# Performance work log

Measured on AMD Instinct MI355X. Metric: run time of the kernel, lower is better.

## Reference

```python
import jax, jax.numpy as jnp
import numpy as np

VOC, EMB, HID = 32000, 512, 1024
B, S = 16, 256


def setup_inputs() -> dict:
    key = jax.random.key(0)
    ks = jax.random.split(key, 12)
    s_e = 1.0 / np.sqrt(HID)
    inp = {
        "inputs": jax.random.randint(ks[0], (B, S), 0, VOC, dtype=jnp.int64),
        "emb": jax.random.normal(ks[1], (VOC, EMB), dtype=jnp.float32),
        "W_ih1": jax.random.uniform(ks[2], (4 * HID, EMB), minval=-s_e, maxval=s_e),
        "W_hh1": jax.random.uniform(ks[3], (4 * HID, HID), minval=-s_e, maxval=s_e),
        "b_ih1": jax.random.uniform(ks[4], (4 * HID,), minval=-s_e, maxval=s_e),
        "b_hh1": jax.random.uniform(ks[5], (4 * HID,), minval=-s_e, maxval=s_e),
        "W_ih2": jax.random.uniform(ks[6], (4 * HID, HID), minval=-s_e, maxval=s_e),
        "W_hh2": jax.random.uniform(ks[7], (4 * HID, HID), minval=-s_e, maxval=s_e),
        "b_ih2": jax.random.uniform(ks[8], (4 * HID,), minval=-s_e, maxval=s_e),
        "b_hh2": jax.random.uniform(ks[9], (4 * HID,), minval=-s_e, maxval=s_e),
        "W_log": jax.random.uniform(ks[10], (VOC, HID), minval=-s_e, maxval=s_e),
        "b_log": jnp.zeros((VOC,), dtype=jnp.float32),  # init_weights zeroes logits bias
    }
    return inp


def _lstm_cell(x, h, c, W_ih, W_hh, b_ih, b_hh):
    # PyTorch LSTMCell: gates ordered (i, f, g, o)
    g = x @ W_ih.T + b_ih + h @ W_hh.T + b_hh  # [B, 4H]
    i, f, gg, o = jnp.split(g, 4, axis=-1)
    c_new = jax.nn.sigmoid(f) * c + jax.nn.sigmoid(i) * jnp.tanh(gg)
    h_new = jax.nn.sigmoid(o) * jnp.tanh(c_new)
    return h_new, c_new


def reference(inputs, emb, W_ih1, W_hh1, b_ih1, b_hh1,
              W_ih2, W_hh2, b_ih2, b_hh2, W_log, b_log):
    # Dropout is evaluated in inference mode (identity), for determinism.
    embed = emb[inputs]  # [B, S, E]
    xs = jnp.swapaxes(embed, 0, 1)  # [S, B, E]
    bsz = inputs.shape[0]
    h1 = jnp.zeros((bsz, HID), embed.dtype)
    c1 = jnp.zeros((bsz, HID), embed.dtype)
    h2 = jnp.zeros((bsz, HID), embed.dtype)
    c2 = jnp.zeros((bsz, HID), embed.dtype)

    def step(carry, x_t):
        h1, c1, h2, c2 = carry
        h1, c1 = _lstm_cell(x_t, h1, c1, W_ih1, W_hh1, b_ih1, b_hh1)
        h2, c2 = _lstm_cell(h1, h2, c2, W_ih2, W_hh2, b_ih2, b_hh2)
        return (h1, c1, h2, c2), h2

    _, hid_seq = jax.lax.scan(step, (h1, c1, h2, c2), xs)  # [S, B, H]
    hid_seq = jnp.swapaxes(hid_seq, 0, 1)  # [B, S, H]
    logits = hid_seq @ W_log.T + b_log  # [B, S, V]
    return jax.nn.log_softmax(logits, axis=-1)
```

## Files before the change

### kernel.cpp

```cpp
#include <hip/hip_runtime.h>
#include <hip/hip_bf16.h>

typedef __attribute__((ext_vector_type(8))) _Float16 half8;
typedef __attribute__((ext_vector_type(4))) _Float16 half4;
typedef __attribute__((ext_vector_type(4))) float f32x4;
typedef __attribute__((ext_vector_type(4))) unsigned int u32x4;

#define VOC 32000
#define EMB 512
#define HID 1024
#define SS  256
#define NROW 4096
#define CHK 43
#define CSTRIDE 64
#define SLOTB (64 * CSTRIDE * 16)
#define NS 4
#define SPIN (1 << 16)
#define ROWH 264

__device__ __forceinline__ float sigf(float x) {
    return 1.f / (1.f + __expf(-x));
}
__device__ __forceinline__ float tanh_c(float x) {
    x = fminf(fmaxf(x, -15.f), 15.f);
    float e = __expf(2.f * x);
    return (e - 1.f) / (e + 1.f);
}

__device__ __forceinline__ u32x4 ldg_u4_cc(const void* p) {
    u32x4 r;
    asm volatile("global_load_dwordx4 %0, %1, off sc0 sc1" : "=v"(r) : "v"(p));
    return r;
}
__device__ __forceinline__ void stg_u4_cc(void* p, u32x4 v) {
    asm volatile("global_store_dwordx4 %0, %1, off sc0 sc1" :: "v"(p), "v"(v) : "memory");
}
__device__ __forceinline__ void stg_u32_cc(unsigned* p, unsigned v) {
    asm volatile("global_store_dword %0, %1, off sc0 sc1" :: "v"(p), "v"(v) : "memory");
}
__device__ __forceinline__ unsigned ldg_u32_cc(const unsigned* p) {
    unsigned v;
    asm volatile("global_load_dword %0, %1, off sc0 sc1\n\ts_waitcnt vmcnt(0)"
                 : "=v"(v) : "v"(p) : "memory");
    return v;
}
__device__ __forceinline__ half8 to_agpr(half8 v) {
    asm volatile("" : "+a"(v));
    return v;
}
__device__ __forceinline__ void gload16(const void* g, void* lds) {
    __builtin_amdgcn_global_load_lds(
        (const __attribute__((address_space(1))) unsigned int*)(uintptr_t)g,
        (__attribute__((address_space(3))) unsigned int*)(unsigned int)(uintptr_t)lds,
        16, 0, 0);
}

__global__ void k_zero(float* p, int n) {
    int i = blockIdx.x * blockDim.x + threadIdx.x;
    int st = gridDim.x * blockDim.x;
    for (; i < n; i += st) p[i] = 0.f;
}

__global__ void k_f32_to_f16(const float* __restrict__ src,
                             _Float16* __restrict__ dst, int n4) {
    int i = blockIdx.x * blockDim.x + threadIdx.x;
    int st = gridDim.x * blockDim.x;
    for (; i < n4; i += st) {
        float4 v = ((const float4*)src)[i];
        half4 o = {(_Float16)v.x, (_Float16)v.y, (_Float16)v.z, (_Float16)v.w};
        ((half4*)dst)[i] = o;
    }
}

__global__ void k_bias(const float* bi1, const float* bh1,
                       const float* bi2, const float* bh2,
                       float* b1, float* b2) {
    int i = blockIdx.x * blockDim.x + threadIdx.x;
    if (i < 4 * HID) { b1[i] = bi1[i] + bh1[i]; b2[i] = bi2[i] + bh2[i]; }
}

__global__ void k_embed(const int* __restrict__ tok, const float* __restrict__ emb,
                        _Float16* __restrict__ A) {
    int idx = blockIdx.x * 256 + threadIdx.x;
    if (idx >= NROW * (EMB / 4)) return;
    int r = idx >> 7, c4 = idx & 127;
    int t = r >> 4, b = r & 15;
    int token = tok[b * SS + t];
    float4 v = ((const float4*)(emb + (size_t)token * EMB))[c4];
    half4 o = {(_Float16)v.x, (_Float16)v.y, (_Float16)v.z, (_Float16)v.w};
    ((half4*)(A + (size_t)r * EMB))[c4] = o;
}

template <int F16OUT>
__global__ __launch_bounds__(256) void k_gemm_bt(
    const _Float16* __restrict__ A, const _Float16* __restrict__ B,
    const float* __restrict__ bias, float* __restrict__ C,
    _Float16* __restrict__ Ch, int M, int N, int K, int scatter, int swz) {
    __shared__ __align__(16) _Float16 As[128 * 32];
    __shared__ __align__(16) _Float16 Bs[128 * 32];
    int tid = threadIdx.x;
    int wave = tid >> 6, lane = tid & 63;
    int nbx = gridDim.x;
    int lin = blockIdx.y * nbx + blockIdx.x;
    if (swz) {
        int n = nbx * gridDim.y, cpx = n >> 3;
        lin = (lin & 7) * cpx + (lin >> 3);
    }
    int bRow = (lin / nbx) * 128, bCol = (lin % nbx) * 128;
    int wr = (wave >> 1) * 64, wc = (wave & 1) * 64;
    f32x4 acc[4][4] = {};

    int lrow = lane & 15, khalf = (lane >> 4) * 8;

    for (int kt = 0; kt < K; kt += 32) {
#pragma unroll
        for (int q = 0; q < 2; ++q) {
            int ci = q * 256 + wave * 64 + lane;
            int row = ci >> 2, c8 = (ci & 3) * 8;
            int ldsoff = (q * 256 + wave * 64) * 16;
            gload16(A + (size_t)(bRow + row) * K + kt + c8, (char*)As + ldsoff);
            gload16(B + (size_t)(bCol + row) * K + kt + c8, (char*)Bs + ldsoff);
        }
        __syncthreads();
        half8 a[4], b[4];
#pragma unroll
        for (int i = 0; i < 4; ++i)
            a[i] = *(const half8*)(&As[(wr + 16 * i + lrow) * 32 + khalf]);
#pragma unroll
        for (int j = 0; j < 4; ++j)
            b[j] = *(const half8*)(&Bs[(wc + 16 * j + lrow) * 32 + khalf]);
#pragma unroll
        for (int i = 0; i < 4; ++i)
#pragma unroll
            for (int j = 0; j < 4; ++j)
                acc[i][j] = __builtin_amdgcn_mfma_f32_16x16x32_f16(a[i], b[j], acc[i][j], 0, 0, 0);
        __syncthreads();
    }

    int lcol = lane & 15, lrow4 = (lane >> 4) * 4;
#pragma unroll
    for (int i = 0; i < 4; ++i)
#pragma unroll
        for (int j = 0; j < 4; ++j)
#pragma unroll
            for (int q = 0; q < 4; ++q) {
                int gr = bRow + wr + 16 * i + lrow4 + q;
                int gc = bCol + wc + 16 * j + lcol;
                float v = acc[i][j][q] + bias[gc];
                size_t orow = scatter ? (size_t)(((gr & 15) << 8) | (gr >> 4)) : (size_t)gr;
                if (F16OUT) Ch[orow * (size_t)N + gc] = (_Float16)v;
                else        C[orow * (size_t)N + gc] = v;
            }
}

__device__ __forceinline__ void poll_stage2(const char* base, int exp, int cnt,
                                            unsigned short* hs, int sbp, int r) {
    u32x4 cv[11];
#pragma unroll
    for (int j = 0; j < 11; ++j)
        if (j < cnt) cv[j] = ldg_u4_cc(base + j * 64);
    for (int it = 0; it < SPIN; ++it) {
        asm volatile("s_waitcnt vmcnt(0)" ::: "memory");
        __builtin_amdgcn_sched_barrier(0);
        bool bad = false;
#pragma unroll
        for (int j = 0; j < 11; ++j)
            if (j < cnt && (int)cv[j][3] < exp) {
                cv[j] = ldg_u4_cc(base + j * 64);
                bad = true;
            }
        if (!bad) break;
        __builtin_amdgcn_s_sleep(1);
    }
#pragma unroll
    for (int j = 0; j < 11; ++j)
        if (j < cnt) {
            int c = r + 4 * j;
            unsigned* dst = (unsigned*)((char*)hs + sbp * (2 * ROWH) + c * 12);
            dst[0] = cv[j][0]; dst[1] = cv[j][1]; dst[2] = cv[j][2];
        }
}

__global__ __launch_bounds__(256, 1) void k_rnn(
    const float* __restrict__ X,
    const _Float16* __restrict__ Whh1,
    const _Float16* __restrict__ Wih2,
    const _Float16* __restrict__ Whh2,
    const float* __restrict__ b2s,
    char* __restrict__ h1buf,
    char* __restrict__ h2buf,
    unsigned* __restrict__ prog,
    _Float16* __restrict__ h2seq) {
    __shared__ __align__(16) unsigned short hsPA[64 * ROWH];
    __shared__ __align__(16) unsigned short hsPB[64 * ROWH];
    __shared__ float gs[4][1024];
    __shared__ __align__(16) unsigned short hstage[264];
    int tid = threadIdx.x;
    int w = tid >> 6, l = tid & 63;
    int bid = blockIdx.x;
    int layer = bid >> 6, sb = bid & 63;
    int sbp = tid >> 2, r = tid & 3;
    int cnt = (r == 3) ? 10 : 11;
    size_t choff = (size_t)(sbp * CSTRIDE + r) * 16;
    int hp = l >> 5;
    int hoff = (l & 15) * 16 + ((l >> 4) & 1) * 8;

    half8 wA[32];
    half8 wB[32];
    {
        const _Float16* base = layer ? Wih2 : Whh1;
        const _Float16* wp = base + (size_t)(w * HID + sb * 16 + (l & 15)) * HID + (l >> 4) * 8;
#pragma unroll
        for (int kt = 0; kt < 32; ++kt)
            wA[kt] = to_agpr(*(const half8*)(wp + kt * 32));
        if (layer) {
            const _Float16* wq = Whh2 + (size_t)(w * HID + sb * 16 + (l & 15)) * HID + (l >> 4) * 8;
#pragma unroll
            for (int kt = 0; kt < 32; ++kt)
                wB[kt] = to_agpr(*(const half8*)(wq + kt * 32));
        }
    }
    float bias_v = layer ? b2s[w * HID + sb * 16 + (l & 15)] : 0.f;

    int eb = tid >> 4, ecol = tid & 15;
    int gidx = ((eb >> 2) * 16 + ecol) * 4 + (eb & 3);
    float creg = 0.f;
    int pc = 0;

    if (!layer) {
        const float* xbase = X + (size_t)w * HID + sb * 16 + (l & 15);
        int bq = (l >> 4) * 4;
        f32x4 xreg;
        {
            const float* xp = xbase + (size_t)bq * 4096;
            xreg[0] = xp[0]; xreg[1] = xp[4096];
            xreg[2] = xp[8192]; xreg[3] = xp[12288];
        }
        for (int g = 0; g < SS; ++g) {
            int tn = (g + 1 < SS) ? g + 1 : SS - 1;
            const float* xp = xbase + (size_t)(tn * 16 + bq) * 4096;
            float xn0 = xp[0], xn1 = xp[4096], xn2 = xp[8192], xn3 = xp[12288];

            poll_stage2(h1buf + ((g - 1) & 3) * SLOTB + choff, g, cnt, hsPA, sbp, r);
            __syncthreads();
            if (tid == 0) stg_u32_cc(prog + (size_t)bid * 16, (unsigned)(g + 1));

            f32x4 a0 = xreg, a1 = {}, a2 = {}, a3 = {};
#pragma unroll
            for (int c = 0; c < 4; ++c) {
                half8 ha[8];
#pragma unroll
                for (int j = 0; j < 8; ++j)
                    ha[j] = *(const half8*)(hsPA + (2 * (c * 8 + j) + hp) * ROWH + hoff);
#pragma unroll
                for (int j = 0; j < 8; ++j) {
                    f32x4* ac = (j & 3) == 0 ? &a0 : (j & 3) == 1 ? &a1 : (j & 3) == 2 ? &a2 : &a3;
                    *ac = __builtin_amdgcn_mfma_f32_16x16x32_f16(ha[j], wA[c * 8 + j], *ac, 0, 0, 0);
                }
            }
            a0 = (a0 + a1) + (a2 + a3);

            *(f32x4*)(&gs[w][l * 4]) = a0;
            __syncthreads();

            float gi = gs[0][gidx], gf = gs[1][gidx], gg = gs[2][gidx], go = gs[3][gidx];
            float cn = sigf(gf) * creg + sigf(gi) * tanh_c(gg);
            float hn = sigf(go) * tanh_c(cn);
            creg = cn;
            _Float16 hh = (_Float16)hn;
            unsigned short hu;
            __builtin_memcpy(&hu, &hh, 2);
            hstage[eb * 16 + ecol] = hu;
            xreg[0] = xn0; xreg[1] = xn1; xreg[2] = xn2; xreg[3] = xn3;
            __syncthreads();

            if (tid < 128 && pc < g - 2) {
                const unsigned* pp = prog + (size_t)tid * 16;
                for (int it = 0; it < SPIN; ++it) {
                    unsigned v = ldg_u32_cc(pp);
                    if ((int)v >= g - 2) { pc = (int)v; break; }
                    __builtin_amdgcn_s_sleep(1);
                }
            }
            __syncthreads();
            if (w == 0 && l < CHK) {
                const unsigned* hsu = (const unsigned*)hstage;
                u32x4 pv;
                pv[0] = hsu[l * 3]; pv[1] = hsu[l * 3 + 1]; pv[2] = hsu[l * 3 + 2];
                pv[3] = (unsigned)(g + 1);
                stg_u4_cc(h1buf + (g & 3) * SLOTB + (size_t)(sb * CSTRIDE + l) * 16, pv);
            }
        }
    } else {
        for (int s = 0; s < SS; ++s) {
            poll_stage2(h2buf + ((s - 1) & 3) * SLOTB + choff, s, cnt, hsPB, sbp, r);
            poll_stage2(h1buf + (s & 3) * SLOTB + choff, s + 1, cnt, hsPA, sbp, r);
            __syncthreads();
            if (tid == 0) stg_u32_cc(prog + (size_t)bid * 16, (unsigned)(s + 1));

            f32x4 a0 = {bias_v, bias_v, bias_v, bias_v}, a1 = {}, a2 = {}, a3 = {};
#pragma unroll
            for (int c = 0; c < 4; ++c) {
                half8 ha[8];
#pragma unroll
                for (int j = 0; j < 8; ++j)
                    ha[j] = *(const half8*)(hsPB + (2 * (c * 8 + j) + hp) * ROWH + hoff);
#pragma unroll
                for (int j = 0; j < 8; ++j) {
                    f32x4* ac = (j & 3) == 0 ? &a0 : (j & 3) == 1 ? &a1 : (j & 3) == 2 ? &a2 : &a3;
                    *ac = __builtin_amdgcn_mfma_f32_16x16x32_f16(ha[j], wB[c * 8 + j], *ac, 0, 0, 0);
                }
            }
#pragma unroll
            for (int c = 0; c < 4; ++c) {
                half8 ha[8];
#pragma unroll
                for (int j = 0; j < 8; ++j)
                    ha[j] = *(const half8*)(hsPA + (2 * (c * 8 + j) + hp) * ROWH + hoff);
#pragma unroll
                for (int j = 0; j < 8; ++j) {
                    f32x4* ac = (j & 3) == 0 ? &a0 : (j & 3) == 1 ? &a1 : (j & 3) == 2 ? &a2 : &a3;
                    *ac = __builtin_amdgcn_mfma_f32_16x16x32_f16(ha[j], wA[c * 8 + j], *ac, 0, 0, 0);
                }
            }
            a0 = (a0 + a1) + (a2 + a3);

            *(f32x4*)(&gs[w][l * 4]) = a0;
            __syncthreads();

            float gi = gs[0][gidx], gf = gs[1][gidx], gg = gs[2][gidx], go = gs[3][gidx];
            float cn = sigf(gf) * creg + sigf(gi) * tanh_c(gg);
            float hn = sigf(go) * tanh_c(cn);
            creg = cn;
            _Float16 hh = (_Float16)hn;
            unsigned short hu;
            __builtin_memcpy(&hu, &hh, 2);
            hstage[eb * 16 + ecol] = hu;
            __syncthreads();

            if (tid < 64 && pc < s - 2) {
                const unsigned* pp = prog + (size_t)(64 + tid) * 16;
                for (int it = 0; it < SPIN; ++it) {
                    unsigned v = ldg_u32_cc(pp);
                    if ((int)v >= s - 2) { pc = (int)v; break; }
                    __builtin_amdgcn_s_sleep(1);
                }
            }
            __syncthreads();
            if (w == 0 && l < CHK) {
                const unsigned* hsu = (const unsigned*)hstage;
                u32x4 pv;
                pv[0] = hsu[l * 3]; pv[1] = hsu[l * 3 + 1]; pv[2] = hsu[l * 3 + 2];
                pv[3] = (unsigned)(s + 1);
                stg_u4_cc(h2buf + (s & 3) * SLOTB + (size_t)(sb * CSTRIDE + l) * 16, pv);
            }
            if (w == 1 && l < 32) {
                half8 hv = *(const half8*)((const char*)hstage + l * 16);
                *(half8*)(h2seq + (size_t)(s * 16 + (l >> 1)) * HID + sb * 16 + (l & 1) * 8) = hv;
            }
        }
    }
}

__global__ __launch_bounds__(320) void k_lsm_f(float* __restrict__ logits) {
    int r = blockIdx.x, tid = threadIdx.x;
    float* row = logits + (size_t)r * VOC;
    f32x4 v[25];
    float m = -3.4e38f;
#pragma unroll
    for (int j = 0; j < 25; ++j) {
        v[j] = ((const f32x4*)row)[tid + 320 * j];
        m = fmaxf(fmaxf(fmaxf(m, v[j][0]), fmaxf(v[j][1], v[j][2])), v[j][3]);
    }
#pragma unroll
    for (int off = 1; off < 64; off <<= 1) m = fmaxf(m, __shfl_xor(m, off));
    __shared__ float sm[5], ssum[5];
    int wv = tid >> 6;
    if ((tid & 63) == 0) sm[wv] = m;
    __syncthreads();
    m = fmaxf(fmaxf(fmaxf(sm[0], sm[1]), fmaxf(sm[2], sm[3])), sm[4]);
    float s = 0.f;
#pragma unroll
    for (int j = 0; j < 25; ++j)
        s += (__expf(v[j][0] - m) + __expf(v[j][1] - m)) +
             (__expf(v[j][2] - m) + __expf(v[j][3] - m));
#pragma unroll
    for (int off = 1; off < 64; off <<= 1) s += __shfl_xor(s, off);
    if ((tid & 63) == 0) ssum[wv] = s;
    __syncthreads();
    s = (ssum[0] + ssum[1]) + (ssum[2] + ssum[3]) + ssum[4];
    float lse = m + __logf(s);
#pragma unroll
    for (int j = 0; j < 25; ++j) {
        f32x4 o = v[j];
        o[0] -= lse; o[1] -= lse; o[2] -= lse; o[3] -= lse;
        ((f32x4*)row)[tid + 320 * j] = o;
    }
}

__global__ __launch_bounds__(320) void k_lsm_h(const _Float16* __restrict__ lg,
                                               float* __restrict__ out) {
    int r = blockIdx.x, tid = threadIdx.x;
    const half4* row = (const half4*)(lg + (size_t)r * VOC);
    float* orow = out + (size_t)r * VOC;
    half4 v[25];
    float m = -3.4e38f;
#pragma unroll
    for (int j = 0; j < 25; ++j) {
        v[j] = row[tid + 320 * j];
        float a = (float)v[j][0], b = (float)v[j][1], c = (float)v[j][2], d = (float)v[j][3];
        m = fmaxf(fmaxf(fmaxf(m, a), fmaxf(b, c)), d);
    }
#pragma unroll
    for (int off = 1; off < 64; off <<= 1) m = fmaxf(m, __shfl_xor(m, off));
    __shared__ float sm[5], ssum[5];
    int wv = tid >> 6;
    if ((tid & 63) == 0) sm[wv] = m;
    __syncthreads();
    m = fmaxf(fmaxf(fmaxf(sm[0], sm[1]), fmaxf(sm[2], sm[3])), sm[4]);
    float s = 0.f;
#pragma unroll
    for (int j = 0; j < 25; ++j)
        s += (__expf((float)v[j][0] - m) + __expf((float)v[j][1] - m)) +
             (__expf((float)v[j][2] - m) + __expf((float)v[j][3] - m));
#pragma unroll
    for (int off = 1; off < 64; off <<= 1) s += __shfl_xor(s, off);
    if ((tid & 63) == 0) ssum[wv] = s;
    __syncthreads();
    s = (ssum[0] + ssum[1]) + (ssum[2] + ssum[3]) + ssum[4];
    float lse = m + __logf(s);
#pragma unroll
    for (int j = 0; j < 25; ++j) {
        f32x4 o = {(float)v[j][0] - lse, (float)v[j][1] - lse,
                   (float)v[j][2] - lse, (float)v[j][3] - lse};
        ((f32x4*)orow)[tid + 320 * j] = o;
    }
}

extern "C" void kernel_launch(void* const* d_in, const int* in_sizes, int n_in,
                              void* d_out, int out_size, void* d_ws, size_t ws_size,
                              hipStream_t stream) {
    const int*   tok   = (const int*)d_in[0];
    const float* emb   = (const float*)d_in[1];
    const float* W_ih1 = (const float*)d_in[2];
    const float* W_hh1 = (const float*)d_in[3];
    const float* b_ih1 = (const float*)d_in[4];
    const float* b_hh1 = (const float*)d_in[5];
    const float* W_ih2 = (const float*)d_in[6];
    const float* W_hh2 = (const float*)d_in[7];
    const float* b_ih2 = (const float*)d_in[8];
    const float* b_hh2 = (const float*)d_in[9];
    const float* W_log = (const float*)d_in[10];
    const float* b_log = (const float*)d_in[11];
    float* out = (float*)d_out;

    char* w = (char*)d_ws;
    auto alloc = [&](size_t bytes) {
        char* p = w;
        w += (bytes + 255) & ~(size_t)255;
        return p;
    };
    _Float16* Wih1h = (_Float16*)alloc((size_t)4096 * 512 * 2);
    _Float16* Whh1h = (_Float16*)alloc((size_t)4096 * 1024 * 2);
    _Float16* Wih2h = (_Float16*)alloc((size_t)4096 * 1024 * 2);
    _Float16* Whh2h = (_Float16*)alloc((size_t)4096 * 1024 * 2);
    _Float16* Wlogh = (_Float16*)alloc((size_t)VOC * 1024 * 2);
    _Float16* Abuf  = (_Float16*)alloc((size_t)4096 * 512 * 2);
    float* X        = (float*)alloc((size_t)4096 * 4096 * 4);
    _Float16* h2seq = (_Float16*)alloc((size_t)4096 * 1024 * 2);
    float* b1s      = (float*)alloc(4096 * 4);
    float* b2s      = (float*)alloc(4096 * 4);
    char* h1buf     = alloc(NS * SLOTB);
    char* h2buf     = alloc(NS * SLOTB);
    unsigned* prog  = (unsigned*)alloc(128 * 64);
    size_t need = (size_t)(w - (char*)d_ws) + (size_t)NROW * VOC * 2;
    _Float16* logh = (need <= ws_size) ? (_Float16*)alloc((size_t)NROW * VOC * 2) : nullptr;

    k_zero<<<64, 256, 0, stream>>>((float*)h1buf, (2 * NS * SLOTB + 128 * 64) / 4);

    k_f32_to_f16<<<2048, 256, 0, stream>>>(W_ih1, Wih1h, 4096 * 512 / 4);
    k_f32_to_f16<<<2048, 256, 0, stream>>>(W_hh1, Whh1h, 4096 * 1024 / 4);
    k_f32_to_f16<<<2048, 256, 0, stream>>>(W_ih2, Wih2h, 4096 * 1024 / 4);
    k_f32_to_f16<<<2048, 256, 0, stream>>>(W_hh2, Whh2h, 4096 * 1024 / 4);
    k_f32_to_f16<<<2048, 256, 0, stream>>>(W_log, Wlogh, VOC * 1024 / 4);
    k_bias<<<16, 256, 0, stream>>>(b_ih1, b_hh1, b_ih2, b_hh2, b1s, b2s);

    k_embed<<<2048, 256, 0, stream>>>(tok, emb, Abuf);
    k_gemm_bt<0><<<dim3(32, 32), 256, 0, stream>>>(Abuf, Wih1h, b1s, X, nullptr,
                                                   4096, 4096, 512, 0, 1);

    k_rnn<<<128, 256, 0, stream>>>(X, Whh1h, Wih2h, Whh2h, b2s,
                                   h1buf, h2buf, prog, h2seq);

    if (logh) {
        k_gemm_bt<1><<<dim3(VOC / 128, 32), 256, 0, stream>>>(h2seq, Wlogh, b_log,
                                                              nullptr, logh,
                                                              4096, VOC, 1024, 1, 1);
        k_lsm_h<<<4096, 320, 0, stream>>>(logh, out);
    } else {
        k_gemm_bt<0><<<dim3(VOC / 128, 32), 256, 0, stream>>>(h2seq, Wlogh, b_log,
                                                              out, nullptr,
                                                              4096, VOC, 1024, 1, 1);
        k_lsm_f<<<4096, 320, 0, stream>>>(out);
    }
}
```

Before: 1.708 ms.

## Overlap layer-2 h1 wait with recurrent MFMA and merge weight conversions

Measured after the change: 1.871 ms. 9.5% more time.

```diff
diff --git a/kernel.cpp b/kernel.cpp
--- a/kernel.cpp
+++ b/kernel.cpp
@@ -61,14 +61,37 @@
     for (; i < n; i += st) p[i] = 0.f;
 }
 
-__global__ void k_f32_to_f16(const float* __restrict__ src,
-                             _Float16* __restrict__ dst, int n4) {
-    int i = blockIdx.x * blockDim.x + threadIdx.x;
-    int st = gridDim.x * blockDim.x;
-    for (; i < n4; i += st) {
-        float4 v = ((const float4*)src)[i];
+__global__ void k_cvt_all(const float* __restrict__ s0, const float* __restrict__ s1,
+                          const float* __restrict__ s2, const float* __restrict__ s3,
+                          const float* __restrict__ s4,
+                          _Float16* __restrict__ d0, _Float16* __restrict__ d1,
+                          _Float16* __restrict__ d2, _Float16* __restrict__ d3,
+                          _Float16* __restrict__ d4) {
+    const int n0 = 4096 * 512 / 4;
+    const int n1 = 4096 * 1024 / 4;
+    const int n4 = VOC * 1024 / 4;
+    const int nT = n0 + 3 * n1 + n4;
+    int i = blockIdx.x * 256 + threadIdx.x;
+    int st = gridDim.x * 256;
+    for (; i < nT; i += st) {
+        const float* s; _Float16* d; int k = i;
+        if (k < n0) { s = s0; d = d0; }
+        else {
+            k -= n0;
+            if (k < n1) { s = s1; d = d1; }
+            else {
+                k -= n1;
+                if (k < n1) { s = s2; d = d2; }
+                else {
+                    k -= n1;
+                    if (k < n1) { s = s3; d = d3; }
+                    else { k -= n1; s = s4; d = d4; }
+                }
+            }
+        }
+        float4 v = ((const float4*)s)[k];
         half4 o = {(_Float16)v.x, (_Float16)v.y, (_Float16)v.z, (_Float16)v.w};
-        ((half4*)dst)[i] = o;
+        ((half4*)d)[k] = o;
     }
 }
 
@@ -153,12 +176,14 @@
             }
 }
 
-__device__ __forceinline__ void poll_stage2(const char* base, int exp, int cnt,
-                                            unsigned short* hs, int sbp, int r) {
-    u32x4 cv[11];
+__device__ __forceinline__ void poll_issue2(const char* base, int cnt, u32x4* cv) {
 #pragma unroll
     for (int j = 0; j < 11; ++j)
         if (j < cnt) cv[j] = ldg_u4_cc(base + j * 64);
+}
+__device__ __forceinline__ void poll_wait_stage(const char* base, int exp, int cnt,
+                                                u32x4* cv, unsigned short* hs,
+                                                int sbp, int r) {
     for (int it = 0; it < SPIN; ++it) {
         asm volatile("s_waitcnt vmcnt(0)" ::: "memory");
         __builtin_amdgcn_sched_barrier(0);
@@ -241,7 +266,12 @@
             const float* xp = xbase + (size_t)(tn * 16 + bq) * 4096;
             float xn0 = xp[0], xn1 = xp[4096], xn2 = xp[8192], xn3 = xp[12288];
 
-            poll_stage2(h1buf + ((g - 1) & 3) * SLOTB + choff, g, cnt, hsPA, sbp, r);
+            {
+                u32x4 cv[11];
+                const char* base = h1buf + ((g - 1) & 3) * SLOTB + choff;
+                poll_issue2(base, cnt, cv);
+                poll_wait_stage(base, g, cnt, cv, hsPA, sbp, r);
+            }
             __syncthreads();
             if (tid == 0) stg_u32_cc(prog + (size_t)bid * 16, (unsigned)(g + 1));
 
@@ -293,10 +323,13 @@
         }
     } else {
         for (int s = 0; s < SS; ++s) {
-            poll_stage2(h2buf + ((s - 1) & 3) * SLOTB + choff, s, cnt, hsPB, sbp, r);
-            poll_stage2(h1buf + (s & 3) * SLOTB + choff, s + 1, cnt, hsPA, sbp, r);
-            __syncthreads();
-            if (tid == 0) stg_u32_cc(prog + (size_t)bid * 16, (unsigned)(s + 1));
+            const char* baseB = h2buf + ((s - 1) & 3) * SLOTB + choff;
+            const char* baseA = h1buf + (s & 3) * SLOTB + choff;
+            u32x4 cvB[11], cvA[11];
+            poll_issue2(baseB, cnt, cvB);
+            poll_issue2(baseA, cnt, cvA);
+            poll_wait_stage(baseB, s, cnt, cvB, hsPB, sbp, r);
+            __syncthreads();
 
             f32x4 a0 = {bias_v, bias_v, bias_v, bias_v}, a1 = {}, a2 = {}, a3 = {};
 #pragma unroll
@@ -311,6 +344,10 @@
                     *ac = __builtin_amdgcn_mfma_f32_16x16x32_f16(ha[j], wB[c * 8 + j], *ac, 0, 0, 0);
                 }
             }
+            poll_wait_stage(baseA, s + 1, cnt, cvA, hsPA, sbp, r);
+            __syncthreads();
+            if (tid == 0) stg_u32_cc(prog + (size_t)bid * 16, (unsigned)(s + 1));
+
 #pragma unroll
             for (int c = 0; c < 4; ++c) {
                 half8 ha[8];
@@ -478,11 +515,8 @@
 
     k_zero<<<64, 256, 0, stream>>>((float*)h1buf, (2 * NS * SLOTB + 128 * 64) / 4);
 
-    k_f32_to_f16<<<2048, 256, 0, stream>>>(W_ih1, Wih1h, 4096 * 512 / 4);
-    k_f32_to_f16<<<2048, 256, 0, stream>>>(W_hh1, Whh1h, 4096 * 1024 / 4);
-    k_f32_to_f16<<<2048, 256, 0, stream>>>(W_ih2, Wih2h, 4096 * 1024 / 4);
-    k_f32_to_f16<<<2048, 256, 0, stream>>>(W_hh2, Whh2h, 4096 * 1024 / 4);
-    k_f32_to_f16<<<2048, 256, 0, stream>>>(W_log, Wlogh, VOC * 1024 / 4);
+    k_cvt_all<<<2048, 256, 0, stream>>>(W_ih1, W_hh1, W_ih2, W_hh2, W_log,
+                                        Wih1h, Whh1h, Wih2h, Whh2h, Wlogh);
     k_bias<<<16, 256, 0, stream>>>(b_ih1, b_hh1, b_ih2, b_hh2, b1s, b2s);
 
     k_embed<<<2048, 256, 0, stream>>>(tok, emb, Abuf);
```
